# Kernel optimization log

Hardware: AMD Instinct MI355X
Metric: run time of the kernel (lower is better)

The kernel has to match this reference:

```python
import jax, jax.numpy as jnp
import numpy as np

B, L, D, H = 8, 2, 2048, 16
HD = D // H
DFF = 4 * D
BS = 16                      # KV-cache block size
SEQ = 2047                   # tokens already cached; +1 new token -> context 2048
CTX = SEQ + 1
MB = (CTX + BS - 1) // BS    # 128 logical blocks per sequence
NB = L * B * MB              # 2048 physical blocks (contiguous allocation)
SCALE = 1.0 / HD ** 0.5
EPS = 1e-5


def setup_inputs() -> dict:
    key = jax.random.key(0)
    ks = jax.random.split(key, 8)
    x = jax.random.normal(ks[0], (B, 1, D), jnp.float32)
    # paged KV heaps (simplified layout [n_blocks, H, block_size, head_dim])
    key_heap = jnp.zeros((NB, H, BS, HD), jnp.float32)
    val_heap = jnp.zeros((NB, H, BS, HD), jnp.float32)
    # contiguous physical-block allocation, matching PagedTransformerData
    bt = np.zeros((L, B, MB), np.int32)
    cur = 0
    for b in range(B):
        for l in range(L):
            bt[l, b] = np.arange(cur, cur + MB)
            cur += MB
    block_tables = jnp.asarray(bt)
    logical, offset = SEQ // BS, SEQ % BS
    slot_mapping = jnp.asarray(bt[:, :, logical].astype(np.int64) * BS + offset)  # [L, B]
    context_lens = jnp.full((B,), CTX, jnp.int32)
    w = lambda k, shape: jax.random.normal(k, shape, jnp.float32) * 0.02
    wq = w(ks[1], (L, D, D)); wk = w(ks[2], (L, D, D))
    wv = w(ks[3], (L, D, D)); wo = w(ks[4], (L, D, D))
    w1 = w(ks[5], (L, DFF, D)); w2 = w(ks[6], (L, D, DFF)); w3 = w(ks[7], (L, DFF, D))
    norm1_w = jnp.ones((L, D), jnp.float32)
    norm2_w = jnp.ones((L, D), jnp.float32)
    final_norm_w = jnp.ones((D,), jnp.float32)
    return dict(x=x, key_heap=key_heap, val_heap=val_heap, block_tables=block_tables,
                slot_mapping=slot_mapping, context_lens=context_lens,
                wq=wq, wk=wk, wv=wv, wo=wo, w1=w1, w2=w2, w3=w3,
                norm1_w=norm1_w, norm2_w=norm2_w, final_norm_w=final_norm_w)


def _rmsnorm(x, w):
    return x * jax.lax.rsqrt(jnp.mean(x * x, axis=-1, keepdims=True) + EPS) * w


def _forward(x, key_heap, val_heap, wq, wk, wv, wo, w1, w2, w3,
             norm1_w, norm2_w, final_norm_w, block_tables, slot_mapping, context_lens):
    t_idx = jnp.arange(MB * BS)
    valid = t_idx[None, :] < context_lens[:, None]          # [B, T]
    for i in range(L):
        res = x
        h = _rmsnorm(x, norm1_w[i])[:, 0]                   # [B, D]
        q = (h @ wq[i].T).reshape(B, H, HD)
        k = (h @ wk[i].T).reshape(B, H, HD)
        v = (h @ wv[i].T).reshape(B, H, HD)
        # reshape_and_cache: scatter new K/V into paged heaps via slot_mapping
        blk = slot_mapping[i] // BS                          # [B]
        off = slot_mapping[i] % BS                           # [B]
        key_heap = key_heap.at[blk, :, off, :].set(k)
        val_heap = val_heap.at[blk, :, off, :].set(v)
        # paged_attention: gather KV blocks via block table
        bt = block_tables[i]                                 # [B, MB]
        K = jnp.swapaxes(key_heap[bt], 2, 3).reshape(B, MB * BS, H, HD)
        V = jnp.swapaxes(val_heap[bt], 2, 3).reshape(B, MB * BS, H, HD)
        s = jnp.einsum('bhd,bthd->bht', q, K) * SCALE
        s = jnp.where(valid[:, None, :], s, jnp.finfo(s.dtype).min)
        p = jax.nn.softmax(s, axis=-1)
        o = jnp.einsum('bht,bthd->bhd', p, V).reshape(B, 1, D)
        x = o @ wo[i].T + res
        # SwiGLU FFN
        res = x
        h = _rmsnorm(x, norm2_w[i])
        x = (jax.nn.silu(h @ w1[i].T) * (h @ w3[i].T)) @ w2[i].T + res
    return _rmsnorm(x, final_norm_w)


def reference(x, key_heap, val_heap, block_tables, slot_mapping, context_lens,
              wq, wk, wv, wo, w1, w2, w3, norm1_w, norm2_w, final_norm_w):
    return _forward(x, key_heap, val_heap, wq, wk, wv, wo, w1, w2, w3,
                    norm1_w, norm2_w, final_norm_w, block_tables, slot_mapping, context_lens)
```

## Files before the change

### kernel.cpp

```cpp
#include <hip/hip_runtime.h>
#include <hip/hip_bf16.h>

constexpr int BB   = 8;
constexpr int LL   = 2;
constexpr int DD   = 2048;
constexpr int HH   = 16;
constexpr int HDIM = 128;
constexpr int DFFN = 8192;
constexpr int BSZ  = 16;
constexpr int MBLK = 128;
constexpr int NSPL = 16;
constexpr int TSPL = 128;
constexpr float EPSR  = 1e-5f;
constexpr float QSCALE = 0.08838834764831845f;

__device__ __forceinline__ bool probe_bf(const unsigned* p){ return p[0] != 0x3F800000u; }

__device__ __forceinline__ float bflo(unsigned u){ return __uint_as_float(u << 16); }
__device__ __forceinline__ float bfhi(unsigned u){ return __uint_as_float(u & 0xffff0000u); }

template<bool BF>
__device__ __forceinline__ const void* eoff(const void* p, size_t off){
  return BF ? (const void*)((const unsigned short*)p + off)
            : (const void*)((const float*)p + off);
}

template<bool BF>
__device__ __forceinline__ float2 ld2(const void* p, int idx){
  if (BF){
    unsigned u = *(const unsigned*)((const unsigned short*)p + idx);
    return make_float2(bflo(u), bfhi(u));
  }
  return *(const float2*)((const float*)p + idx);
}

template<bool BF>
__device__ __forceinline__ float wave_dot(const void* pw, const float* __restrict__ v,
                                          int n, int lane){
  float acc = 0.f;
  if (BF){
    const unsigned short* w = (const unsigned short*)pw;
    for (int base = lane*8; base < n; base += 512){
      uint4 wp  = *reinterpret_cast<const uint4*>(w + base);
      float4 v0 = *reinterpret_cast<const float4*>(v + base);
      float4 v1 = *reinterpret_cast<const float4*>(v + base + 4);
      acc += v0.x*bflo(wp.x) + v0.y*bfhi(wp.x);
      acc += v0.z*bflo(wp.y) + v0.w*bfhi(wp.y);
      acc += v1.x*bflo(wp.z) + v1.y*bfhi(wp.z);
      acc += v1.z*bflo(wp.w) + v1.w*bfhi(wp.w);
    }
  } else {
    const float* w = (const float*)pw;
    for (int base = lane*8; base < n; base += 512){
      float4 w0 = *reinterpret_cast<const float4*>(w + base);
      float4 w1 = *reinterpret_cast<const float4*>(w + base + 4);
      float4 v0 = *reinterpret_cast<const float4*>(v + base);
      float4 v1 = *reinterpret_cast<const float4*>(v + base + 4);
      acc += v0.x*w0.x + v0.y*w0.y + v0.z*w0.z + v0.w*w0.w;
      acc += v1.x*w1.x + v1.y*w1.y + v1.z*w1.z + v1.w*w1.w;
    }
  }
  return acc;
}

__device__ __forceinline__ float wave_reduce_down(float a){
  #pragma unroll
  for (int off = 32; off > 0; off >>= 1) a += __shfl_down(a, off);
  return a;
}
__device__ __forceinline__ float wave_reduce_xor(float a){
  #pragma unroll
  for (int m = 1; m < 64; m <<= 1) a += __shfl_xor(a, m);
  return a;
}

template<bool BF>
__device__ void init_x_body(const void* x, float* X){
  int i = blockIdx.x*blockDim.x + threadIdx.x;
  if (i < BB*DD){
    X[i] = BF ? __uint_as_float(((unsigned)((const unsigned short*)x)[i]) << 16)
              : ((const float*)x)[i];
  }
}
__global__ void k_init_x(const unsigned* probe, const void* x, float* X){
  if (probe_bf(probe)) init_x_body<true>(x, X); else init_x_body<false>(x, X);
}

template<bool BF>
__device__ void rmsnorm_body(const float* x, const void* w, size_t woff, float* h){
  int b = blockIdx.x, tid = threadIdx.x;
  const float* xb = x + b*DD;
  const void* wb = eoff<BF>(w, woff);
  float acc = 0.f;
  for (int idx = tid*4; idx < DD; idx += 1024){
    float4 v = *reinterpret_cast<const float4*>(xb + idx);
    acc += v.x*v.x + v.y*v.y + v.z*v.z + v.w*v.w;
  }
  __shared__ float red[256];
  red[tid] = acc; __syncthreads();
  for (int s = 128; s > 0; s >>= 1){ if (tid < s) red[tid] += red[tid+s]; __syncthreads(); }
  float rs = rsqrtf(red[0]/(float)DD + EPSR);
  for (int idx = tid*2; idx < DD; idx += 512){
    float2 wv = ld2<BF>(wb, idx);
    float2 xv = *reinterpret_cast<const float2*>(xb + idx);
    float2 hv; hv.x = xv.x*rs*wv.x; hv.y = xv.y*rs*wv.y;
    *reinterpret_cast<float2*>(h + b*DD + idx) = hv;
  }
}
__global__ void k_rmsnorm(const unsigned* probe, const float* x, const void* w, size_t woff,
                          float* h){
  if (probe_bf(probe)) rmsnorm_body<true>(x, w, woff, h);
  else                 rmsnorm_body<false>(x, w, woff, h);
}

template<bool BF>
__device__ void final_body(const float* x, const void* w, void* out){
  int b = blockIdx.x, tid = threadIdx.x;
  const float* xb = x + b*DD;
  float acc = 0.f;
  for (int idx = tid*4; idx < DD; idx += 1024){
    float4 v = *reinterpret_cast<const float4*>(xb + idx);
    acc += v.x*v.x + v.y*v.y + v.z*v.z + v.w*v.w;
  }
  __shared__ float red[256];
  red[tid] = acc; __syncthreads();
  for (int s = 128; s > 0; s >>= 1){ if (tid < s) red[tid] += red[tid+s]; __syncthreads(); }
  float rs = rsqrtf(red[0]/(float)DD + EPSR);
  for (int idx = tid*2; idx < DD; idx += 512){
    float2 wv = ld2<BF>(w, idx);
    float2 xv = *reinterpret_cast<const float2*>(xb + idx);
    float r0 = xv.x*rs*wv.x, r1 = xv.y*rs*wv.y;
    if (BF){
      __hip_bfloat16* o = (__hip_bfloat16*)out;
      o[b*DD + idx]     = __float2bfloat16(r0);
      o[b*DD + idx + 1] = __float2bfloat16(r1);
    } else {
      float* o = (float*)out;
      o[b*DD + idx] = r0; o[b*DD + idx + 1] = r1;
    }
  }
}
__global__ void k_final(const unsigned* probe, const float* x, const void* w, void* out){
  if (probe_bf(probe)) final_body<true>(x, w, out);
  else                 final_body<false>(x, w, out);
}

template<bool BF>
__device__ void qkv_body(const float* h, const void* wq, const void* wk, const void* wv,
                         size_t woff, float* q, float* k, float* v){
  int wid  = (blockIdx.x*blockDim.x + threadIdx.x) >> 6;
  int lane = threadIdx.x & 63;
  int which = wid >> 14;
  int rem   = wid & 16383;
  int b = rem >> 11, j = rem & 2047;
  const void* w = eoff<BF>(which == 0 ? wq : which == 1 ? wk : wv, woff + (size_t)j*DD);
  float acc = wave_dot<BF>(w, h + b*DD, DD, lane);
  acc = wave_reduce_down(acc);
  if (lane == 0){
    float* dst = (which == 0 ? q : which == 1 ? k : v);
    dst[b*DD + j] = acc;
  }
}
__global__ void k_qkv(const unsigned* probe, const float* h, const void* wq, const void* wk,
                      const void* wv, size_t woff, float* q, float* k, float* v){
  if (probe_bf(probe)) qkv_body<true>(h, wq, wk, wv, woff, q, k, v);
  else                 qkv_body<false>(h, wq, wk, wv, woff, q, k, v);
}

template<bool BF>
__device__ void attn_body(const float* Q, const float* Kn, const float* Vn,
                          const void* kh, const void* vh,
                          const int* bt, const int* ctx_lens, float* part){
  int bid = blockIdx.x;
  int s = bid & (NSPL-1);
  int hh = (bid >> 4) & (HH-1);
  int b = bid >> 8;
  int tid = threadIdx.x;
  int w = tid >> 6, lane = tid & 63;
  int ctx = ctx_lens[b];
  int t0 = s*TSPL, tend = min(t0 + TSPL, ctx);
  int voff = b*DD + hh*HDIM + 2*lane;
  float q0 = Q[voff]*QSCALE, q1 = Q[voff+1]*QSCALE;
  float m = -INFINITY, l = 0.f, o0 = 0.f, o1 = 0.f;
  const int* btb = bt + b*MBLK;
  for (int t = t0 + w; t < tend; t += 4){
    float k0, k1, v0, v1;
    if (t == ctx - 1){
      k0 = Kn[voff]; k1 = Kn[voff+1];
      v0 = Vn[voff]; v1 = Vn[voff+1];
    } else {
      int blk = btb[t >> 4];
      int base = ((blk*HH + hh)*BSZ + (t & 15))*HDIM + 2*lane;
      float2 kv = ld2<BF>(kh, base);
      float2 vv = ld2<BF>(vh, base);
      k0 = kv.x; k1 = kv.y; v0 = vv.x; v1 = vv.y;
    }
    float sc = wave_reduce_xor(q0*k0 + q1*k1);
    float mn = fmaxf(m, sc);
    float co = __expf(m - mn);
    float p  = __expf(sc - mn);
    l  = l*co + p;
    o0 = o0*co + p*v0;
    o1 = o1*co + p*v1;
    m = mn;
  }
  __shared__ float sm[4], sl[4], so[4][128];
  if (lane == 0){ sm[w] = m; sl[w] = l; }
  so[w][2*lane] = o0; so[w][2*lane+1] = o1;
  __syncthreads();
  if (tid < 128){
    int d = tid;
    float ms = fmaxf(fmaxf(sm[0], sm[1]), fmaxf(sm[2], sm[3]));
    float num = 0.f, den = 0.f;
    if (ms > -INFINITY){
      #pragma unroll
      for (int ww = 0; ww < 4; ww++){
        if (sm[ww] > -INFINITY){
          float e = __expf(sm[ww] - ms);
          num += e*so[ww][d];
          den += e*sl[ww];
        }
      }
    }
    int pidx = ((b*HH + hh)*NSPL + s)*130;
    if (d == 0){ part[pidx] = ms; part[pidx+1] = den; }
    part[pidx + 2 + d] = num;
  }
}
__global__ void k_attn_partial(const unsigned* probe, const float* Q, const float* Kn,
                               const float* Vn, const void* kh, const void* vh,
                               const int* bt, const int* ctx_lens, float* part){
  if (probe_bf(probe)) attn_body<true>(Q, Kn, Vn, kh, vh, bt, ctx_lens, part);
  else                 attn_body<false>(Q, Kn, Vn, kh, vh, bt, ctx_lens, part);
}

__global__ void k_attn_combine(const float* __restrict__ part, float* __restrict__ O){
  int bid = blockIdx.x;
  int d = threadIdx.x;
  float ms = -INFINITY;
  #pragma unroll
  for (int s = 0; s < NSPL; s++) ms = fmaxf(ms, part[(bid*NSPL + s)*130]);
  float num = 0.f, den = 0.f;
  #pragma unroll
  for (int s = 0; s < NSPL; s++){
    float msv = part[(bid*NSPL + s)*130];
    if (msv > -INFINITY){
      float e = __expf(msv - ms);
      den += e*part[(bid*NSPL + s)*130 + 1];
      num += e*part[(bid*NSPL + s)*130 + 2 + d];
    }
  }
  O[bid*HDIM + d] = num/den;
}

template<bool BF>
__device__ void gemv_res_body(const float* vec, const void* w, size_t woff, float* x, int n){
  int wid  = (blockIdx.x*blockDim.x + threadIdx.x) >> 6;
  int lane = threadIdx.x & 63;
  int b = wid >> 11, j = wid & 2047;
  float acc = wave_dot<BF>(eoff<BF>(w, woff + (size_t)j*n), vec + b*n, n, lane);
  acc = wave_reduce_down(acc);
  if (lane == 0) x[b*DD + j] += acc;
}
__global__ void k_gemv_res(const unsigned* probe, const float* vec, const void* w, size_t woff,
                           float* x, int n){
  if (probe_bf(probe)) gemv_res_body<true>(vec, w, woff, x, n);
  else                 gemv_res_body<false>(vec, w, woff, x, n);
}

template<bool BF>
__device__ void ffn13_body(const float* h, const void* w1, const void* w3, size_t woff,
                           float* g){
  int wid  = (blockIdx.x*blockDim.x + threadIdx.x) >> 6;
  int lane = threadIdx.x & 63;
  int b = wid >> 13, j = wid & 8191;
  const float* hb = h + b*DD;
  float a = wave_dot<BF>(eoff<BF>(w1, woff + (size_t)j*DD), hb, DD, lane);
  float c = wave_dot<BF>(eoff<BF>(w3, woff + (size_t)j*DD), hb, DD, lane);
  a = wave_reduce_down(a);
  c = wave_reduce_down(c);
  if (lane == 0) g[b*DFFN + j] = (a/(1.f + __expf(-a)))*c;
}
__global__ void k_ffn13(const unsigned* probe, const float* h, const void* w1, const void* w3,
                        size_t woff, float* g){
  if (probe_bf(probe)) ffn13_body<true>(h, w1, w3, woff, g);
  else                 ffn13_body<false>(h, w1, w3, woff, g);
}

extern "C" void kernel_launch(void* const* d_in, const int* in_sizes, int n_in,
                              void* d_out, int out_size, void* d_ws, size_t ws_size,
                              hipStream_t stream) {
  const void* x_in     = d_in[0];
  const void* key_heap = d_in[1];
  const void* val_heap = d_in[2];
  const int* block_tables = (const int*)d_in[3];
  const int* context_lens = (const int*)d_in[5];
  const void* wq = d_in[6],  *wk = d_in[7],  *wv = d_in[8],  *wo = d_in[9];
  const void* w1 = d_in[10], *w2 = d_in[11], *w3 = d_in[12];
  const void* n1 = d_in[13], *n2 = d_in[14], *fn = d_in[15];
  const unsigned* probe = (const unsigned*)d_in[13];
  void* out = d_out;

  float* ws  = (float*)d_ws;
  float* X   = ws;
  float* Hb  = ws + 16384;
  float* Qw  = ws + 32768;
  float* Kw  = ws + 49152;
  float* Vw  = ws + 65536;
  float* Ow  = ws + 81920;
  float* G   = ws + 98304;
  float* PART= ws + 163840;

  k_init_x<<<64, 256, 0, stream>>>(probe, x_in, X);
  for (int l = 0; l < LL; l++){
    k_rmsnorm<<<BB, 256, 0, stream>>>(probe, X, n1, (size_t)l*DD, Hb);
    k_qkv<<<12288, 256, 0, stream>>>(probe, Hb, wq, wk, wv, (size_t)l*DD*DD, Qw, Kw, Vw);
    k_attn_partial<<<BB*HH*NSPL, 256, 0, stream>>>(probe, Qw, Kw, Vw, key_heap, val_heap,
                                                   block_tables + l*BB*MBLK, context_lens, PART);
    k_attn_combine<<<BB*HH, 128, 0, stream>>>(PART, Ow);
    k_gemv_res<<<4096, 256, 0, stream>>>(probe, Ow, wo, (size_t)l*DD*DD, X, DD);
    k_rmsnorm<<<BB, 256, 0, stream>>>(probe, X, n2, (size_t)l*DD, Hb);
    k_ffn13<<<16384, 256, 0, stream>>>(probe, Hb, w1, w3, (size_t)l*DFFN*DD, G);
    k_gemv_res<<<4096, 256, 0, stream>>>(probe, G, w2, (size_t)l*DD*DFFN, X, DFFN);
  }
  k_final<<<BB, 256, 0, stream>>>(probe, X, fn, out);
}
```

Baseline: 1.273 ms.

## Batch GEMVs across all sequences with LDS-staged activations and fused RMSNorm

Replaces the one-wave-per-(batch,row) GEMV kernels with batched kernels. Each wave loads a few weight rows once and multiplies them against all 8 batch vectors, which are staged in 64KB of shared memory. This removes the eightfold weight re-reads that previously depended on L2 hits. RMSNorm is fused into the QKV and W1/W3 kernels, and the W2 projection uses split-K over four chunks with atomicAdd into the residual. The trade-offs are small grids (128–512 blocks), large LDS use per block that limits occupancy, and float atomics that make the W2 accumulation order nondeterministic.

```diff
diff --git a/kernel.cpp b/kernel.cpp
--- a/kernel.cpp
+++ b/kernel.cpp
@@ -35,32 +35,12 @@
 }
 
 template<bool BF>
-__device__ __forceinline__ float wave_dot(const void* pw, const float* __restrict__ v,
-                                          int n, int lane){
-  float acc = 0.f;
+__device__ __forceinline__ float4 ld4(const void* p, int idx){
   if (BF){
-    const unsigned short* w = (const unsigned short*)pw;
-    for (int base = lane*8; base < n; base += 512){
-      uint4 wp  = *reinterpret_cast<const uint4*>(w + base);
-      float4 v0 = *reinterpret_cast<const float4*>(v + base);
-      float4 v1 = *reinterpret_cast<const float4*>(v + base + 4);
-      acc += v0.x*bflo(wp.x) + v0.y*bfhi(wp.x);
-      acc += v0.z*bflo(wp.y) + v0.w*bfhi(wp.y);
-      acc += v1.x*bflo(wp.z) + v1.y*bfhi(wp.z);
-      acc += v1.z*bflo(wp.w) + v1.w*bfhi(wp.w);
-    }
-  } else {
-    const float* w = (const float*)pw;
-    for (int base = lane*8; base < n; base += 512){
-      float4 w0 = *reinterpret_cast<const float4*>(w + base);
-      float4 w1 = *reinterpret_cast<const float4*>(w + base + 4);
-      float4 v0 = *reinterpret_cast<const float4*>(v + base);
-      float4 v1 = *reinterpret_cast<const float4*>(v + base + 4);
-      acc += v0.x*w0.x + v0.y*w0.y + v0.z*w0.z + v0.w*w0.w;
-      acc += v1.x*w1.x + v1.y*w1.y + v1.z*w1.z + v1.w*w1.w;
-    }
-  }
-  return acc;
+    uint2 u = *(const uint2*)((const unsigned short*)p + idx);
+    return make_float4(bflo(u.x), bfhi(u.x), bflo(u.y), bfhi(u.y));
+  }
+  return *(const float4*)((const float*)p + idx);
 }
 
 __device__ __forceinline__ float wave_reduce_down(float a){
@@ -84,33 +64,6 @@
 }
 __global__ void k_init_x(const unsigned* probe, const void* x, float* X){
   if (probe_bf(probe)) init_x_body<true>(x, X); else init_x_body<false>(x, X);
-}
-
-template<bool BF>
-__device__ void rmsnorm_body(const float* x, const void* w, size_t woff, float* h){
-  int b = blockIdx.x, tid = threadIdx.x;
-  const float* xb = x + b*DD;
-  const void* wb = eoff<BF>(w, woff);
-  float acc = 0.f;
-  for (int idx = tid*4; idx < DD; idx += 1024){
-    float4 v = *reinterpret_cast<const float4*>(xb + idx);
-    acc += v.x*v.x + v.y*v.y + v.z*v.z + v.w*v.w;
-  }
-  __shared__ float red[256];
-  red[tid] = acc; __syncthreads();
-  for (int s = 128; s > 0; s >>= 1){ if (tid < s) red[tid] += red[tid+s]; __syncthreads(); }
-  float rs = rsqrtf(red[0]/(float)DD + EPSR);
-  for (int idx = tid*2; idx < DD; idx += 512){
-    float2 wv = ld2<BF>(wb, idx);
-    float2 xv = *reinterpret_cast<const float2*>(xb + idx);
-    float2 hv; hv.x = xv.x*rs*wv.x; hv.y = xv.y*rs*wv.y;
-    *reinterpret_cast<float2*>(h + b*DD + idx) = hv;
-  }
-}
-__global__ void k_rmsnorm(const unsigned* probe, const float* x, const void* w, size_t woff,
-                          float* h){
-  if (probe_bf(probe)) rmsnorm_body<true>(x, w, woff, h);
-  else                 rmsnorm_body<false>(x, w, woff, h);
 }
 
 template<bool BF>
@@ -145,26 +98,188 @@
   else                 final_body<false>(x, w, out);
 }
 
-template<bool BF>
-__device__ void qkv_body(const float* h, const void* wq, const void* wk, const void* wv,
-                         size_t woff, float* q, float* k, float* v){
-  int wid  = (blockIdx.x*blockDim.x + threadIdx.x) >> 6;
-  int lane = threadIdx.x & 63;
-  int which = wid >> 14;
-  int rem   = wid & 16383;
-  int b = rem >> 11, j = rem & 2047;
-  const void* w = eoff<BF>(which == 0 ? wq : which == 1 ? wk : wv, woff + (size_t)j*DD);
-  float acc = wave_dot<BF>(w, h + b*DD, DD, lane);
-  acc = wave_reduce_down(acc);
-  if (lane == 0){
-    float* dst = (which == 0 ? q : which == 1 ? k : v);
-    dst[b*DD + j] = acc;
-  }
-}
-__global__ void k_qkv(const unsigned* probe, const float* h, const void* wq, const void* wk,
-                      const void* wv, size_t woff, float* q, float* k, float* v){
-  if (probe_bf(probe)) qkv_body<true>(h, wq, wk, wv, woff, q, k, v);
-  else                 qkv_body<false>(h, wq, wk, wv, woff, q, k, v);
+
+template<bool BF>
+__device__ __forceinline__ void stage_rms(const float* __restrict__ X, const void* nw,
+                                          size_t noff, float* hs){
+  int w = threadIdx.x >> 6, lane = threadIdx.x & 63;
+  const float* xb = X + w*DD;
+  float acc = 0.f;
+  #pragma unroll
+  for (int it = 0, idx = lane*4; it < 8; ++it, idx += 256){
+    float4 v = *(const float4*)(xb + idx);
+    acc += v.x*v.x + v.y*v.y + v.z*v.z + v.w*v.w;
+  }
+  acc = wave_reduce_xor(acc);
+  float rs = rsqrtf(acc/(float)DD + EPSR);
+  const void* wb = eoff<BF>(nw, noff);
+  #pragma unroll
+  for (int it = 0, idx = lane*4; it < 8; ++it, idx += 256){
+    float4 v  = *(const float4*)(xb + idx);
+    float4 wv = ld4<BF>(wb, idx);
+    float4 hv = make_float4(v.x*rs*wv.x, v.y*rs*wv.y, v.z*rs*wv.z, v.w*rs*wv.w);
+    *(float4*)(hs + w*DD + idx) = hv;
+  }
+}
+
+__device__ __forceinline__ void stage_raw(const float* __restrict__ src, float* hs){
+  int tid = threadIdx.x;
+  for (int i = tid*4; i < 8*DD; i += 2048)
+    *(float4*)(hs + i) = *(const float4*)(src + i);
+}
+
+__device__ __forceinline__ void stage_raw_g(const float* __restrict__ G, int chunk, float* hs){
+  int tid = threadIdx.x;
+  for (int i = tid*4; i < 8*DD; i += 2048){
+    int b = i >> 11, d = i & 2047;
+    *(float4*)(hs + i) = *(const float4*)(G + b*DFFN + chunk*2048 + d);
+  }
+}
+
+template<bool BF, int R>
+__device__ __forceinline__ void gemv_rows(const void* wbase, size_t rowStride,
+                                          const float* hs, int lane, float acc[][8]){
+  #pragma unroll
+  for (int it = 0, base = lane*4; it < 4; ++it, base += 256){
+    float wf[R][8];
+    #pragma unroll
+    for (int r = 0; r < R; r++){
+      if (BF){
+        const unsigned short* rp = (const unsigned short*)wbase + (size_t)r*rowStride;
+        uint2 wa = *(const uint2*)(rp + base);
+        uint2 wb = *(const uint2*)(rp + base + 1024);
+        wf[r][0]=bflo(wa.x); wf[r][1]=bfhi(wa.x); wf[r][2]=bflo(wa.y); wf[r][3]=bfhi(wa.y);
+        wf[r][4]=bflo(wb.x); wf[r][5]=bfhi(wb.x); wf[r][6]=bflo(wb.y); wf[r][7]=bfhi(wb.y);
+      } else {
+        const float* rp = (const float*)wbase + (size_t)r*rowStride;
+        float4 wa = *(const float4*)(rp + base);
+        float4 wb = *(const float4*)(rp + base + 1024);
+        wf[r][0]=wa.x; wf[r][1]=wa.y; wf[r][2]=wa.z; wf[r][3]=wa.w;
+        wf[r][4]=wb.x; wf[r][5]=wb.y; wf[r][6]=wb.z; wf[r][7]=wb.w;
+      }
+    }
+    #pragma unroll
+    for (int b = 0; b < 8; b++){
+      const float* hb = hs + b*DD + base;
+      float4 h0 = *(const float4*)hb;
+      float4 h1 = *(const float4*)(hb + 1024);
+      #pragma unroll
+      for (int r = 0; r < R; r++){
+        acc[r][b] += h0.x*wf[r][0] + h0.y*wf[r][1] + h0.z*wf[r][2] + h0.w*wf[r][3]
+                   + h1.x*wf[r][4] + h1.y*wf[r][5] + h1.z*wf[r][6] + h1.w*wf[r][7];
+      }
+    }
+  }
+}
+
+template<bool BF>
+__device__ void qkvb_body(const float* X, const void* n1, size_t noff,
+                          const void* wq, const void* wk, const void* wv, size_t woff,
+                          float* Q, float* Ko, float* V){
+  __shared__ float hs[8*DD];
+  stage_rms<BF>(X, n1, noff, hs);
+  __syncthreads();
+  int w = threadIdx.x >> 6, lane = threadIdx.x & 63;
+  int row0 = blockIdx.x*32 + w*4;
+  int which = row0 >> 11;
+  int j0 = row0 & 2047;
+  const void* wm = which == 0 ? wq : which == 1 ? wk : wv;
+  const void* wbase = eoff<BF>(wm, woff + (size_t)j0*DD);
+  float acc[4][8] = {};
+  gemv_rows<BF,4>(wbase, DD, hs, lane, acc);
+  float* dst = which == 0 ? Q : which == 1 ? Ko : V;
+  #pragma unroll
+  for (int r = 0; r < 4; r++)
+    #pragma unroll
+    for (int b = 0; b < 8; b++){
+      float a = wave_reduce_down(acc[r][b]);
+      if (lane == 0) dst[b*DD + j0 + r] = a;
+    }
+}
+__global__ __launch_bounds__(512, 4)
+void k_qkvb(const unsigned* probe, const float* X, const void* n1, size_t noff,
+            const void* wq, const void* wk, const void* wv, size_t woff,
+            float* Q, float* Ko, float* V){
+  if (probe_bf(probe)) qkvb_body<true>(X, n1, noff, wq, wk, wv, woff, Q, Ko, V);
+  else                 qkvb_body<false>(X, n1, noff, wq, wk, wv, woff, Q, Ko, V);
+}
+
+template<bool BF>
+__device__ void wob_body(const float* Ow, const void* wo, size_t woff, float* X){
+  __shared__ float hs[8*DD];
+  stage_raw(Ow, hs);
+  __syncthreads();
+  int w = threadIdx.x >> 6, lane = threadIdx.x & 63;
+  int row0 = blockIdx.x*16 + w*2;
+  const void* wbase = eoff<BF>(wo, woff + (size_t)row0*DD);
+  float acc[2][8] = {};
+  gemv_rows<BF,2>(wbase, DD, hs, lane, acc);
+  #pragma unroll
+  for (int r = 0; r < 2; r++)
+    #pragma unroll
+    for (int b = 0; b < 8; b++){
+      float a = wave_reduce_down(acc[r][b]);
+      if (lane == 0) X[b*DD + row0 + r] += a;
+    }
+}
+__global__ __launch_bounds__(512, 4)
+void k_wob(const unsigned* probe, const float* Ow, const void* wo, size_t woff, float* X){
+  if (probe_bf(probe)) wob_body<true>(Ow, wo, woff, X);
+  else                 wob_body<false>(Ow, wo, woff, X);
+}
+
+template<bool BF>
+__device__ void ffn13b_body(const float* X, const void* n2, size_t noff,
+                            const void* w1, const void* w3, size_t woff, float* G){
+  __shared__ float hs[8*DD];
+  stage_rms<BF>(X, n2, noff, hs);
+  __syncthreads();
+  int w = threadIdx.x >> 6, lane = threadIdx.x & 63;
+  int row0 = blockIdx.x*16 + w*2;
+  const void* w1b = eoff<BF>(w1, woff + (size_t)row0*DD);
+  const void* w3b = eoff<BF>(w3, woff + (size_t)row0*DD);
+  float a1[2][8] = {}, a3[2][8] = {};
+  gemv_rows<BF,2>(w1b, DD, hs, lane, a1);
+  gemv_rows<BF,2>(w3b, DD, hs, lane, a3);
+  #pragma unroll
+  for (int r = 0; r < 2; r++)
+    #pragma unroll
+    for (int b = 0; b < 8; b++){
+      float fa = wave_reduce_down(a1[r][b]);
+      float fc = wave_reduce_down(a3[r][b]);
+      if (lane == 0) G[b*DFFN + row0 + r] = (fa/(1.f + __expf(-fa)))*fc;
+    }
+}
+__global__ __launch_bounds__(512, 4)
+void k_ffn13b(const unsigned* probe, const float* X, const void* n2, size_t noff,
+              const void* w1, const void* w3, size_t woff, float* G){
+  if (probe_bf(probe)) ffn13b_body<true>(X, n2, noff, w1, w3, woff, G);
+  else                 ffn13b_body<false>(X, n2, noff, w1, w3, woff, G);
+}
+
+template<bool BF>
+__device__ void w2b_body(const float* G, const void* w2, size_t woff, float* X){
+  __shared__ float hs[8*DD];
+  int tile = blockIdx.x >> 2, chunk = blockIdx.x & 3;
+  stage_raw_g(G, chunk, hs);
+  __syncthreads();
+  int w = threadIdx.x >> 6, lane = threadIdx.x & 63;
+  int row0 = tile*32 + w*4;
+  const void* wbase = eoff<BF>(w2, woff + (size_t)row0*DFFN + (size_t)chunk*2048);
+  float acc[4][8] = {};
+  gemv_rows<BF,4>(wbase, DFFN, hs, lane, acc);
+  #pragma unroll
+  for (int r = 0; r < 4; r++)
+    #pragma unroll
+    for (int b = 0; b < 8; b++){
+      float a = wave_reduce_down(acc[r][b]);
+      if (lane == 0) atomicAdd(&X[b*DD + row0 + r], a);
+    }
+}
+__global__ __launch_bounds__(512, 4)
+void k_w2b(const unsigned* probe, const float* G, const void* w2, size_t woff, float* X){
+  if (probe_bf(probe)) w2b_body<true>(G, w2, woff, X);
+  else                 w2b_body<false>(G, w2, woff, X);
 }
 
 template<bool BF>
@@ -253,40 +368,6 @@
   O[bid*HDIM + d] = num/den;
 }
 
-template<bool BF>
-__device__ void gemv_res_body(const float* vec, const void* w, size_t woff, float* x, int n){
-  int wid  = (blockIdx.x*blockDim.x + threadIdx.x) >> 6;
-  int lane = threadIdx.x & 63;
-  int b = wid >> 11, j = wid & 2047;
-  float acc = wave_dot<BF>(eoff<BF>(w, woff + (size_t)j*n), vec + b*n, n, lane);
-  acc = wave_reduce_down(acc);
-  if (lane == 0) x[b*DD + j] += acc;
-}
-__global__ void k_gemv_res(const unsigned* probe, const float* vec, const void* w, size_t woff,
-                           float* x, int n){
-  if (probe_bf(probe)) gemv_res_body<true>(vec, w, woff, x, n);
-  else                 gemv_res_body<false>(vec, w, woff, x, n);
-}
-
-template<bool BF>
-__device__ void ffn13_body(const float* h, const void* w1, const void* w3, size_t woff,
-                           float* g){
-  int wid  = (blockIdx.x*blockDim.x + threadIdx.x) >> 6;
-  int lane = threadIdx.x & 63;
-  int b = wid >> 13, j = wid & 8191;
-  const float* hb = h + b*DD;
-  float a = wave_dot<BF>(eoff<BF>(w1, woff + (size_t)j*DD), hb, DD, lane);
-  float c = wave_dot<BF>(eoff<BF>(w3, woff + (size_t)j*DD), hb, DD, lane);
-  a = wave_reduce_down(a);
-  c = wave_reduce_down(c);
-  if (lane == 0) g[b*DFFN + j] = (a/(1.f + __expf(-a)))*c;
-}
-__global__ void k_ffn13(const unsigned* probe, const float* h, const void* w1, const void* w3,
-                        size_t woff, float* g){
-  if (probe_bf(probe)) ffn13_body<true>(h, w1, w3, woff, g);
-  else                 ffn13_body<false>(h, w1, w3, woff, g);
-}
-
 extern "C" void kernel_launch(void* const* d_in, const int* in_sizes, int n_in,
                               void* d_out, int out_size, void* d_ws, size_t ws_size,
                               hipStream_t stream) {
@@ -303,7 +384,6 @@
 
   float* ws  = (float*)d_ws;
   float* X   = ws;
-  float* Hb  = ws + 16384;
   float* Qw  = ws + 32768;
   float* Kw  = ws + 49152;
   float* Vw  = ws + 65536;
@@ -313,15 +393,15 @@
 
   k_init_x<<<64, 256, 0, stream>>>(probe, x_in, X);
   for (int l = 0; l < LL; l++){
-    k_rmsnorm<<<BB, 256, 0, stream>>>(probe, X, n1, (size_t)l*DD, Hb);
-    k_qkv<<<12288, 256, 0, stream>>>(probe, Hb, wq, wk, wv, (size_t)l*DD*DD, Qw, Kw, Vw);
+    k_qkvb<<<192, 512, 0, stream>>>(probe, X, n1, (size_t)l*DD,
+                                    wq, wk, wv, (size_t)l*DD*DD, Qw, Kw, Vw);
     k_attn_partial<<<BB*HH*NSPL, 256, 0, stream>>>(probe, Qw, Kw, Vw, key_heap, val_heap,
                                                    block_tables + l*BB*MBLK, context_lens, PART);
     k_attn_combine<<<BB*HH, 128, 0, stream>>>(PART, Ow);
-    k_gemv_res<<<4096, 256, 0, stream>>>(probe, Ow, wo, (size_t)l*DD*DD, X, DD);
-    k_rmsnorm<<<BB, 256, 0, stream>>>(probe, X, n2, (size_t)l*DD, Hb);
-    k_ffn13<<<16384, 256, 0, stream>>>(probe, Hb, w1, w3, (size_t)l*DFFN*DD, G);
-    k_gemv_res<<<4096, 256, 0, stream>>>(probe, G, w2, (size_t)l*DD*DFFN, X, DFFN);
+    k_wob<<<128, 512, 0, stream>>>(probe, Ow, wo, (size_t)l*DD*DD, X);
+    k_ffn13b<<<512, 512, 0, stream>>>(probe, X, n2, (size_t)l*DD,
+                                      w1, w3, (size_t)l*DFFN*DD, G);
+    k_w2b<<<256, 512, 0, stream>>>(probe, G, w2, (size_t)l*DD*DFFN, X);
   }
   k_final<<<BB, 256, 0, stream>>>(probe, X, fn, out);
 }
```

Measured after the change: 1.458 ms. 1.14x slower.
